# Optimization experiments

Measured on AMD Instinct MI355X. Metric: run time of the kernel, lower is better.

The kernel has to match this reference:

```python
import jax, jax.numpy as jnp
import numpy as np

EPS = 1e-8
NUM_HEADS = 8
SCALE = 25.0
SIM_THRESH = 0.75
BLOCK = 10  # per-frame proposal group size used by the zeroing mask


def _l2norm(x):
    return x / (jnp.linalg.norm(x, axis=-1, keepdims=True) + EPS)


def setup_inputs() -> dict:
    key = jax.random.key(0)
    ks = jax.random.split(key, 7)
    B, N, C = 1, 2000, 256
    H = NUM_HEADS
    x_cls = jax.random.normal(ks[0], (B, N, C), dtype=jnp.float32)
    x_reg = jax.random.normal(ks[1], (B, N, C), dtype=jnp.float32)
    cls_score = jax.random.uniform(ks[2], (N,), dtype=jnp.float32)
    fg_score = jax.random.uniform(ks[3], (N,), dtype=jnp.float32)
    coord_attn = jax.random.uniform(ks[4], (B, H, N, N), dtype=jnp.float32)
    W_qkv_cls = jax.random.normal(ks[5], (3 * C, C), dtype=jnp.float32) * 0.02
    W_qkv_reg = jax.random.normal(ks[6], (3 * C, C), dtype=jnp.float32) * 0.02
    return {"x_cls": x_cls, "x_reg": x_reg, "cls_score": cls_score,
            "fg_score": fg_score, "coord_attn": coord_attn,
            "W_qkv_cls": W_qkv_cls, "W_qkv_reg": W_qkv_reg}


def reference(x_cls, x_reg, cls_score, fg_score, coord_attn, W_qkv_cls, W_qkv_reg):
    B, N, C = x_cls.shape
    H = NUM_HEADS
    D = C // H

    def qkv(x, W):
        t = (x @ W.T).reshape(B, N, 3, H, D).transpose(2, 0, 3, 1, 4)  # [3,B,H,N,D]
        return t[0], t[1], t[2]

    q_cls, k_cls, v_cls = qkv(x_cls, W_qkv_cls)
    q_reg, k_reg, v_reg = qkv(x_reg, W_qkv_reg)

    q_cls, k_cls = _l2norm(q_cls), _l2norm(k_cls)
    q_reg, k_reg = _l2norm(q_reg), _l2norm(k_reg)
    v_cls_normed = _l2norm(v_cls)

    cs = cls_score.reshape(1, 1, 1, N)  # broadcast over [B,H,N,N]
    fs = fg_score.reshape(1, 1, 1, N)

    attn_cls_raw = jnp.einsum('bhnd,bhmd->bhnm', v_cls_normed, v_cls_normed)

    attn_cls = jax.nn.softmax(jnp.einsum('bhnd,bhmd->bhnm', q_cls, k_cls) * SCALE * cs, axis=-1)
    attn_reg = jax.nn.softmax(jnp.einsum('bhnd,bhmd->bhnm', q_reg, k_reg) * SCALE * fs, axis=-1)

    attn = (attn_reg + attn_cls) * 0.5 * coord_attn
    attn = jax.lax.stop_gradient(attn)  # original detaches before masking

    # block-diagonal zeroing: row j zeros cols [j//10*10, j//10*10+9), keep diagonal
    rows = jnp.arange(N)[:, None]
    cols = jnp.arange(N)[None, :]
    block_start = (rows // BLOCK) * BLOCK
    zero_mask = (cols >= block_start) & (cols < block_start + (BLOCK - 1)) & (cols != rows)
    attn = jnp.where(zero_mask, 0.0, attn)

    x = jnp.einsum('bhnm,bhmd->bhnd', attn, v_cls).transpose(0, 2, 1, 3).reshape(B, N, C)
    x_ori = v_cls.transpose(0, 2, 1, 3).reshape(B, N, C)
    x_cat = jnp.concatenate([x, x_ori], axis=-1)  # [B,N,2C]

    # ave=True branch
    sim_raw = jnp.sum(attn_cls_raw, axis=1)[0] / H          # [N,N]
    sim_mask = (sim_raw > SIM_THRESH).astype(x_cls.dtype)
    sim_attn = jnp.sum(attn, axis=1)[0] / H                 # [N,N]
    sim_round2 = jax.nn.softmax(sim_attn, axis=-1)
    sim_round2 = sim_mask * sim_round2 / (jnp.sum(sim_mask * sim_round2, axis=-1, keepdims=True) + EPS)
    return x_cat, sim_round2
```

## Files before the change

### kernel.cpp

```cpp
#include <hip/hip_runtime.h>
#include <math.h>

typedef _Float16 half8 __attribute__((ext_vector_type(8)));
typedef _Float16 half4 __attribute__((ext_vector_type(4)));
typedef float f32x4 __attribute__((ext_vector_type(4)));

constexpr int N = 2000;
constexpr int NP = 2048;
constexpr int H = 8;
constexpr int D = 32;
constexpr float SCL = 25.0f;
constexpr float L2E = 1.4426950408889634f;
constexpr float FM2 = 25.0f * L2E;

#define MFMA16(a,b,c)  __builtin_amdgcn_mfma_f32_16x16x32_f16((a),(b),(c),0,0,0)
#define MFMA16K(a,b,c) __builtin_amdgcn_mfma_f32_16x16x16f16((a),(b),(c),0,0,0)

__device__ __forceinline__ float fexp2(float x) { return __builtin_amdgcn_exp2f(x); }


__global__ __launch_bounds__(256) void wconv_kernel(
    const float* __restrict__ Wc, const float* __restrict__ Wr,
    _Float16* __restrict__ Wch, _Float16* __restrict__ Wrh)
{
    const int i = blockIdx.x * 256 + threadIdx.x;
    Wch[i] = (_Float16)Wc[i];
    Wrh[i] = (_Float16)Wr[i];
}

__global__ __launch_bounds__(256) void qkv_kernel(
    const float* __restrict__ xc, const float* __restrict__ xr,
    const _Float16* __restrict__ Wch, const _Float16* __restrict__ Wrh,
    const float* __restrict__ clsScore, const float* __restrict__ fgScore,
    _Float16* __restrict__ Qch, _Float16* __restrict__ Kch,
    _Float16* __restrict__ Qrh, _Float16* __restrict__ Krh,
    _Float16* __restrict__ Vnh, _Float16* __restrict__ Vth,
    float* __restrict__ out)
{
    constexpr int XS = 264;
    __shared__ _Float16 xs[16 * XS];
    const int t = threadIdx.x;
    const int n0 = blockIdx.x * 16;
    const int by = blockIdx.y;
    const int which = (by < 3) ? by : (by - 3);
    const bool isCls = by < 3;
    const float* x = isCls ? xc : xr;
    const _Float16* Wh = isCls ? Wch : Wrh;

    #pragma unroll
    for (int it = 0; it < 4; ++it) {
        const int f = t + it * 256;
        const int row = f >> 6, c4 = f & 63;
        const float4 v = *(const float4*)(x + (size_t)(n0 + row) * 256 + c4 * 4);
        half4 hv; hv[0]=(_Float16)v.x; hv[1]=(_Float16)v.y; hv[2]=(_Float16)v.z; hv[3]=(_Float16)v.w;
        *(half4*)&xs[row * XS + c4 * 4] = hv;
    }
    __syncthreads();

    const int w = t >> 6, l = t & 63;
    const int lr = l & 15, lg = l >> 4;
    const int obase = which * 256 + w * 64;
    f32x4 acc[4] = {{0,0,0,0},{0,0,0,0},{0,0,0,0},{0,0,0,0}};
    for (int k0 = 0; k0 < 256; k0 += 32) {
        const half8 aX = *(const half8*)&xs[lr * XS + k0 + lg * 8];
        #pragma unroll
        for (int s = 0; s < 4; ++s) {
            const half8 bW = *(const half8*)(Wh + (size_t)(obase + s * 16 + lr) * 256 + k0 + lg * 8);
            acc[s] = MFMA16(aX, bW, acc[s]);
        }
    }
    f32x4 kscale = {1.f,1.f,1.f,1.f};
    if (which == 1) {
        const float* sp = isCls ? clsScore : fgScore;
        kscale = (SCL * L2E) * *(const f32x4*)(sp + n0 + lg*4);
    }
    #pragma unroll
    for (int p = 0; p < 2; ++p) {
        const int h = 2 * w + p;
        float ss[4];
        #pragma unroll
        for (int j = 0; j < 4; ++j) {
            float v = acc[2*p][j]*acc[2*p][j] + acc[2*p+1][j]*acc[2*p+1][j];
            #pragma unroll
            for (int off = 1; off < 16; off <<= 1) v += __shfl_xor(v, off);
            ss[j] = sqrtf(v) + 1e-8f;
        }
        if (which < 2) {
            _Float16* Qd = isCls ? (which == 0 ? Qch : Kch) : (which == 0 ? Qrh : Krh);
            #pragma unroll
            for (int sh = 0; sh < 2; ++sh)
                #pragma unroll
                for (int j = 0; j < 4; ++j)
                    Qd[((size_t)h*NP + n0 + lg*4 + j)*D + sh*16 + lr]
                        = (_Float16)(acc[2*p+sh][j] / ss[j] * kscale[j]);
        } else {
            #pragma unroll
            for (int sh = 0; sh < 2; ++sh) {
                const int d = sh * 16 + lr;
                half4 tv;
                #pragma unroll
                for (int j = 0; j < 4; ++j) {
                    const float raw = acc[2*p+sh][j];
                    Vnh[((size_t)h*NP + n0 + lg*4 + j)*D + d] = (_Float16)(raw / ss[j]);
                    out[(size_t)(n0 + lg*4 + j)*512 + 256 + h*D + d] = raw;
                    tv[j] = (_Float16)raw;
                }
                *(half4*)(Vth + ((size_t)h*D + d)*NP + n0 + lg*4) = tv;
            }
        }
    }
}

__global__ __launch_bounds__(512) void stats_kernel(
    const _Float16* __restrict__ Qch, const _Float16* __restrict__ Kch,
    const _Float16* __restrict__ Qrh, const _Float16* __restrict__ Krh,
    float* __restrict__ BIAS)
{
    __shared__ float Ssh[2][4][16];
    const int t = threadIdx.x;
    const int w = t >> 6, l = t & 63;
    const int nsub = w >> 2, mq = w & 3;
    const int n0 = blockIdx.x * 32 + nsub * 16;
    const int h = blockIdx.y, z = blockIdx.z;
    const _Float16* Q = z ? Qrh : Qch;
    const _Float16* K = z ? Krh : Kch;
    const int lr = l & 15, lg = l >> 4;
    const half8 aQ = *(const half8*)(Q + ((size_t)h*NP + n0 + lr)*D + lg*8);
    float S[4] = {0.f, 0.f, 0.f, 0.f};
    const int mqB0 = (mq == 0) ? 0 : 31*mq;
    const int mqB1 = (mq == 3) ? 125 : 31*(mq+1);
    half8 bK = *(const half8*)(K + ((size_t)h*NP + mqB0*16 + lr)*D + lg*8);
    for (int ms = mqB0; ms < mqB1; ++ms) {
        const half8 cur = bK;
        if (ms + 1 < mqB1)
            bK = *(const half8*)(K + ((size_t)h*NP + (ms+1)*16 + lr)*D + lg*8);
        f32x4 z4 = {0.f, 0.f, 0.f, 0.f};
        const f32x4 c = MFMA16(aQ, cur, z4);
        #pragma unroll
        for (int j = 0; j < 4; ++j) S[j] += fexp2(c[j] - FM2);
    }
    #pragma unroll
    for (int j = 0; j < 4; ++j) {
        #pragma unroll
        for (int off = 1; off < 16; off <<= 1) S[j] += __shfl_xor(S[j], off);
    }
    if (lr == 0) {
        #pragma unroll
        for (int j = 0; j < 4; ++j) Ssh[nsub][mq][lg*4 + j] = S[j];
    }
    __syncthreads();
    if (t < 32) {
        const int ns = t >> 4, rl = t & 15;
        const int n = blockIdx.x * 32 + ns*16 + rl;
        BIAS[((size_t)z*H + h)*NP + n]
            = -__log2f(Ssh[ns][0][rl] + Ssh[ns][1][rl] + Ssh[ns][2][rl] + Ssh[ns][3][rl]) - FM2 - 1.0f;
    }
}

__global__ __launch_bounds__(256) void vvmask_kernel(
    const _Float16* __restrict__ Vnh, unsigned char* __restrict__ Mask)
{
    const int t = threadIdx.x;
    const int w = t >> 6, l = t & 63;
    const int n0 = blockIdx.y * 16;
    const int m00 = blockIdx.x * 256 + w * 64;
    const int lr = l & 15, lg = l >> 4;
    half8 aV[8];
    #pragma unroll
    for (int h = 0; h < 8; ++h)
        aV[h] = *(const half8*)(Vnh + ((size_t)(h*NP + n0 + lr))*D + lg*8);
    for (int s = 0; s < 4; ++s) {
        const int mb = m00 + s*16;
        f32x4 acc = {0.f, 0.f, 0.f, 0.f};
        #pragma unroll
        for (int h = 0; h < 8; ++h) {
            const half8 bV = *(const half8*)(Vnh + ((size_t)(h*NP + mb + lr))*D + lg*8);
            acc = MFMA16(aV[h], bV, acc);
        }
        const int m = mb + lr;
        if (m < N) {
            #pragma unroll
            for (int j = 0; j < 4; ++j) {
                const int n = n0 + lg*4 + j;
                Mask[(size_t)n*N + m] = (acc[j]*0.125f > 0.75f) ? (unsigned char)1 : (unsigned char)0;
            }
        }
    }
}

__global__ __launch_bounds__(256) void attn_kernel(
    const _Float16* __restrict__ Kch, const _Float16* __restrict__ Krh,
    const _Float16* __restrict__ Qch, const _Float16* __restrict__ Qrh,
    const _Float16* __restrict__ Vth, const float* __restrict__ coord,
    const float* __restrict__ BIAS,
    _Float16* __restrict__ SIMH8, float* __restrict__ out)
{
    constexpr int CW = 264;
    __shared__ float costage[2][16][CW];
    __shared__ float pvred[4][2][16][17];

    const int t = threadIdx.x;
    const int w = t >> 6, l = t & 63;
    const int lr = l & 15, lg = l >> 4;
    const int ny = blockIdx.x;
    const int h  = blockIdx.y;
    const int n0 = ny * 16;
    const int n  = n0 + lr;
    const int bs = (n / 10) * 10;

    const half8 aQc = *(const half8*)(Qch + ((size_t)h*NP + n)*D + lg*8);
    const half8 aQr = *(const half8*)(Qrh + ((size_t)h*NP + n)*D + lg*8);
    const float bC = BIAS[(size_t)h*NP + n];
    const float bR = BIAS[(size_t)(H + h)*NP + n];

    f32x4 streg[4];
    auto LOADCH = [&](int c) {
        #pragma unroll
        for (int i = 0; i < 4; ++i) {
            const int g = t + 256*i;
            const int row = g >> 6, c4 = g & 63;
            const int col = c*256 + c4*4;
            if (col < 2000)
                streg[i] = __builtin_nontemporal_load(
                    (const f32x4*)(coord + ((size_t)h*N + n0 + row)*N + col));
            else
                streg[i] = (f32x4){0.f,0.f,0.f,0.f};
        }
    };
    auto WRITECH = [&](int buf) {
        #pragma unroll
        for (int i = 0; i < 4; ++i) {
            const int g = t + 256*i;
            const int row = g >> 6, c4 = g & 63;
            *(f32x4*)&costage[buf][row][c4*4] = streg[i];
        }
    };

    f32x4 pv0 = {0,0,0,0}, pv1 = {0,0,0,0};

    LOADCH(0);
    WRITECH(0);
    __syncthreads();
    int buf = 0;

    for (int c = 0; c < 8; ++c) {
        const bool more = (c + 1 < 8);
        if (more) LOADCH(c + 1);
        __builtin_amdgcn_sched_barrier(0);

        const int nls = (c < 7) ? 4 : ((w < 3) ? 4 : 1);

        half8 kc[4], kr[4]; half4 v0[4], v1[4];
        #pragma unroll
        for (int i = 0; i < 4; ++i) {
            if (i >= nls) break;
            const int s = c*16 + w*4 + i;
            const int m = s*16;
            const size_t kb = ((size_t)h*NP + m + lr)*D + lg*8;
            kc[i] = *(const half8*)(Kch + kb);
            kr[i] = *(const half8*)(Krh + kb);
            v0[i] = *(const half4*)(Vth + ((size_t)(h*D + lr))*NP + m + lg*4);
            v1[i] = *(const half4*)(Vth + ((size_t)(h*D + 16 + lr))*NP + m + lg*4);
        }
        __builtin_amdgcn_sched_barrier(0);

        #pragma unroll
        for (int i = 0; i < 4; ++i) {
            if (i >= nls) break;
            const int s = c*16 + w*4 + i;
            const f32x4 co = *(const f32x4*)&costage[buf][lr][(w*4 + i)*16 + lg*4];
            f32x4 z4 = {0,0,0,0};
            const f32x4 cc = MFMA16(kc[i], aQc, z4);
            const f32x4 cr = MFMA16(kr[i], aQr, z4);
            half4 af;
            #pragma unroll
            for (int j = 0; j < 4; ++j) {
                const int m = s*16 + lg*4 + j;
                float a = (fexp2(cc[j] + bC) + fexp2(cr[j] + bR)) * co[j];
                if (m >= bs && m < bs + 9 && m != n) a = 0.f;
                af[j] = (_Float16)a;
            }
            *(half4*)(SIMH8 + ((size_t)h*N + n)*N + s*16 + lg*4) = af;
            pv0 = MFMA16K(af, v0[i], pv0);
            pv1 = MFMA16K(af, v1[i], pv1);
        }

        if (more) WRITECH(buf ^ 1);
        __syncthreads();
        buf ^= 1;
    }

    #pragma unroll
    for (int j = 0; j < 4; ++j) {
        pvred[w][0][lr][lg*4 + j] = pv0[j];
        pvred[w][1][lr][lg*4 + j] = pv1[j];
    }
    __syncthreads();
    {
        const int e0 = 2*t;
        const int d = e0 & 15, db = (e0 >> 4) & 1, q = e0 >> 5;
        const float u0 = pvred[0][db][d][q]   + pvred[1][db][d][q]
                       + pvred[2][db][d][q]   + pvred[3][db][d][q];
        const float u1 = pvred[0][db][d+1][q] + pvred[1][db][d+1][q]
                       + pvred[2][db][d+1][q] + pvred[3][db][d+1][q];
        *(float2*)(out + (size_t)(n0 + q)*512 + h*32 + db*16 + d) = make_float2(u0, u1);
    }
}

__global__ __launch_bounds__(256) void simfinal_kernel(
    const _Float16* __restrict__ SIMH8, const unsigned char* __restrict__ Mask,
    float* __restrict__ out)
{
    __shared__ float redA[4], redB[4];
    const int n = blockIdx.x, t = threadIdx.x;
    const unsigned char* mrow = Mask + (size_t)n * N;
    const bool act = t < 250;
    float f[8] = {0,0,0,0,0,0,0,0};
    unsigned int mk0 = 0, mk1 = 0;
    float mx = -1e30f;
    if (act) {
        #pragma unroll
        for (int h = 0; h < 8; ++h) {
            const half8 v8 = *(const half8*)(SIMH8 + ((size_t)h*N + n)*N + t*8);
            #pragma unroll
            for (int k = 0; k < 8; ++k) f[k] += (float)v8[k];
        }
        const uint2 mm = *(const uint2*)(mrow + t*8);
        mk0 = mm.x; mk1 = mm.y;
        #pragma unroll
        for (int k = 0; k < 8; ++k) mx = fmaxf(mx, f[k]);
    }
    #pragma unroll
    for (int off = 1; off < 64; off <<= 1) mx = fmaxf(mx, __shfl_xor(mx, off));
    const int wv = t >> 6;
    if ((t & 63) == 0) redA[wv] = mx;
    __syncthreads();
    const float M = fmaxf(fmaxf(redA[0], redA[1]), fmaxf(redA[2], redA[3]));
    float e[8];
    float sA = 0.f, sM = 0.f;
    if (act) {
        #pragma unroll
        for (int k = 0; k < 8; ++k) {
            e[k] = fexp2((f[k] - M) * (L2E * 0.125f));
            sA += e[k];
            const unsigned int mkb = ((k < 4 ? mk0 : mk1) >> (8*(k & 3))) & 0xffu;
            if (mkb) sM += e[k]; else e[k] = 0.f;
        }
    }
    #pragma unroll
    for (int off = 1; off < 64; off <<= 1) { sA += __shfl_xor(sA, off); sM += __shfl_xor(sM, off); }
    __syncthreads();
    if ((t & 63) == 0) { redA[wv] = sA; redB[wv] = sM; }
    __syncthreads();
    const float SA = redA[0] + redA[1] + redA[2] + redA[3];
    const float SMK = redB[0] + redB[1] + redB[2] + redB[3];
    const float inv = 1.f / (SMK + 1e-8f * SA);
    if (act) {
        float* orow = out + 1024000 + (size_t)n*N + t*8;
        *(float4*)(orow)     = make_float4(e[0]*inv, e[1]*inv, e[2]*inv, e[3]*inv);
        *(float4*)(orow + 4) = make_float4(e[4]*inv, e[5]*inv, e[6]*inv, e[7]*inv);
    }
}

extern "C" void kernel_launch(void* const* d_in, const int* in_sizes, int n_in,
                              void* d_out, int out_size, void* d_ws, size_t ws_size,
                              hipStream_t stream) {
    const float* x_cls     = (const float*)d_in[0];
    const float* x_reg     = (const float*)d_in[1];
    const float* cls_score = (const float*)d_in[2];
    const float* fg_score  = (const float*)d_in[3];
    const float* coord     = (const float*)d_in[4];
    const float* Wc        = (const float*)d_in[5];
    const float* Wr        = (const float*)d_in[6];

    char* base = (char*)d_ws;
    float* BIAS      = (float*)base;
    _Float16* SIMH8  = (_Float16*)(base + 131072);
    _Float16* Qch    = (_Float16*)(base + 64131072);
    _Float16* Kch    = Qch + 524288;
    _Float16* Qrh    = Qch + 2*524288;
    _Float16* Krh    = Qch + 3*524288;
    _Float16* Vnh    = Qch + 4*524288;
    _Float16* Vth    = Qch + 5*524288;
    _Float16* Wch    = (_Float16*)(base + 70422528);
    _Float16* Wrh    = (_Float16*)(base + 70815744);
    unsigned char* Mask = (unsigned char*)(base + 71208960);
    float* out = (float*)d_out;

    wconv_kernel<<<768, 256, 0, stream>>>(Wc, Wr, Wch, Wrh);
    qkv_kernel<<<dim3(125, 5), 256, 0, stream>>>(x_cls, x_reg, Wch, Wrh, cls_score, fg_score,
                                                 Qch, Kch, Qrh, Krh, Vnh, Vth, out);
    stats_kernel<<<dim3(63, 8, 2), 512, 0, stream>>>(Qch, Kch, Qrh, Krh, BIAS);
    vvmask_kernel<<<dim3(8, 125), 256, 0, stream>>>(Vnh, Mask);
    attn_kernel<<<dim3(125, 8), 256, 0, stream>>>(Kch, Krh, Qch, Qrh, Vth, coord,
                                                  BIAS, SIMH8, out);
    simfinal_kernel<<<2000, 256, 0, stream>>>(SIMH8, Mask, out);
}
```

Before: 145.0 us.

## Process four heads per attention block and pre-sum head groups before the sim write

Each attn_kernel block now handles four heads instead of one. It sums the masked attention over those heads in registers and writes 2 head-group partial sums to the workspace instead of 8 per-head fp16 matrices, which cuts global write traffic and the simfinal read traffic by about 4x. The coord tile is converted to fp16 when staged in shared memory, so it takes less LDS. In exchange the grid shrinks from 1000 to 250 blocks, register pressure rises (16 coord regs, 4 heads' Q and accumulators), and the coord values lose precision.

```diff
diff --git a/kernel.cpp b/kernel.cpp
--- a/kernel.cpp
+++ b/kernel.cpp
@@ -193,50 +193,63 @@
     const _Float16* __restrict__ Qch, const _Float16* __restrict__ Qrh,
     const _Float16* __restrict__ Vth, const float* __restrict__ coord,
     const float* __restrict__ BIAS,
-    _Float16* __restrict__ SIMH8, float* __restrict__ out)
+    _Float16* __restrict__ SIMG, float* __restrict__ out)
 {
     constexpr int CW = 264;
-    __shared__ float costage[2][16][CW];
-    __shared__ float pvred[4][2][16][17];
+    __shared__ _Float16 costage[2][4][16 * CW];
 
     const int t = threadIdx.x;
     const int w = t >> 6, l = t & 63;
     const int lr = l & 15, lg = l >> 4;
     const int ny = blockIdx.x;
-    const int h  = blockIdx.y;
+    const int g  = blockIdx.y;
+    const int h0 = g * 4;
     const int n0 = ny * 16;
     const int n  = n0 + lr;
     const int bs = (n / 10) * 10;
 
-    const half8 aQc = *(const half8*)(Qch + ((size_t)h*NP + n)*D + lg*8);
-    const half8 aQr = *(const half8*)(Qrh + ((size_t)h*NP + n)*D + lg*8);
-    const float bC = BIAS[(size_t)h*NP + n];
-    const float bR = BIAS[(size_t)(H + h)*NP + n];
-
-    f32x4 streg[4];
+    half8 aQc[4], aQr[4]; float bC[4], bR[4];
+    #pragma unroll
+    for (int hl = 0; hl < 4; ++hl) {
+        const int h = h0 + hl;
+        aQc[hl] = *(const half8*)(Qch + ((size_t)h*NP + n)*D + lg*8);
+        aQr[hl] = *(const half8*)(Qrh + ((size_t)h*NP + n)*D + lg*8);
+        bC[hl]  = BIAS[(size_t)h*NP + n];
+        bR[hl]  = BIAS[(size_t)(H + h)*NP + n];
+    }
+
+    half4 creg[16];
     auto LOADCH = [&](int c) {
         #pragma unroll
-        for (int i = 0; i < 4; ++i) {
-            const int g = t + 256*i;
-            const int row = g >> 6, c4 = g & 63;
-            const int col = c*256 + c4*4;
-            if (col < 2000)
-                streg[i] = __builtin_nontemporal_load(
-                    (const f32x4*)(coord + ((size_t)h*N + n0 + row)*N + col));
-            else
-                streg[i] = (f32x4){0.f,0.f,0.f,0.f};
+        for (int hl = 0; hl < 4; ++hl) {
+            #pragma unroll
+            for (int i = 0; i < 4; ++i) {
+                const int g16 = t + 256*i;
+                const int row = g16 >> 6, c4 = g16 & 63;
+                const int col = c*256 + c4*4;
+                f32x4 v = {0.f,0.f,0.f,0.f};
+                if (col < 2000)
+                    v = *(const f32x4*)(coord + ((size_t)(h0 + hl)*N + n0 + row)*N + col);
+                half4 hv; hv[0]=(_Float16)v[0]; hv[1]=(_Float16)v[1];
+                hv[2]=(_Float16)v[2]; hv[3]=(_Float16)v[3];
+                creg[hl*4 + i] = hv;
+            }
         }
     };
     auto WRITECH = [&](int buf) {
         #pragma unroll
-        for (int i = 0; i < 4; ++i) {
-            const int g = t + 256*i;
-            const int row = g >> 6, c4 = g & 63;
-            *(f32x4*)&costage[buf][row][c4*4] = streg[i];
+        for (int hl = 0; hl < 4; ++hl) {
+            #pragma unroll
+            for (int i = 0; i < 4; ++i) {
+                const int g16 = t + 256*i;
+                const int row = g16 >> 6, c4 = g16 & 63;
+                *(half4*)&costage[buf][hl][row*CW + c4*4] = creg[hl*4 + i];
+            }
         }
     };
 
-    f32x4 pv0 = {0,0,0,0}, pv1 = {0,0,0,0};
+    f32x4 pv0[4] = {{0,0,0,0},{0,0,0,0},{0,0,0,0},{0,0,0,0}};
+    f32x4 pv1[4] = {{0,0,0,0},{0,0,0,0},{0,0,0,0},{0,0,0,0}};
 
     LOADCH(0);
     WRITECH(0);
@@ -250,39 +263,55 @@
 
         const int nls = (c < 7) ? 4 : ((w < 3) ? 4 : 1);
 
-        half8 kc[4], kr[4]; half4 v0[4], v1[4];
+        float sacc[4][4] = {{0,0,0,0},{0,0,0,0},{0,0,0,0},{0,0,0,0}};
+
+        #pragma unroll
+        for (int hl = 0; hl < 4; ++hl) {
+            const int h = h0 + hl;
+            half8 kc[4], kr[4]; half4 v0[4], v1[4];
+            #pragma unroll
+            for (int i = 0; i < 4; ++i) {
+                if (i >= nls) break;
+                const int s = c*16 + w*4 + i;
+                const int m = s*16;
+                const size_t kb = ((size_t)h*NP + m + lr)*D + lg*8;
+                kc[i] = *(const half8*)(Kch + kb);
+                kr[i] = *(const half8*)(Krh + kb);
+                v0[i] = *(const half4*)(Vth + ((size_t)(h*D + lr))*NP + m + lg*4);
+                v1[i] = *(const half4*)(Vth + ((size_t)(h*D + 16 + lr))*NP + m + lg*4);
+            }
+            __builtin_amdgcn_sched_barrier(0);
+
+            #pragma unroll
+            for (int i = 0; i < 4; ++i) {
+                if (i >= nls) break;
+                const int s = c*16 + w*4 + i;
+                const half4 coh = *(const half4*)&costage[buf][hl][lr*CW + (w*4 + i)*16 + lg*4];
+                f32x4 z4 = {0,0,0,0};
+                const f32x4 cc = MFMA16(kc[i], aQc[hl], z4);
+                const f32x4 cr = MFMA16(kr[i], aQr[hl], z4);
+                half4 af;
+                #pragma unroll
+                for (int j = 0; j < 4; ++j) {
+                    const int m = s*16 + lg*4 + j;
+                    float a = (fexp2(cc[j] + bC[hl]) + fexp2(cr[j] + bR[hl])) * (float)coh[j];
+                    if (m >= bs && m < bs + 9 && m != n) a = 0.f;
+                    sacc[i][j] += a;
+                    af[j] = (_Float16)a;
+                }
+                pv0[hl] = MFMA16K(af, v0[i], pv0[hl]);
+                pv1[hl] = MFMA16K(af, v1[i], pv1[hl]);
+            }
+        }
+
         #pragma unroll
         for (int i = 0; i < 4; ++i) {
             if (i >= nls) break;
             const int s = c*16 + w*4 + i;
-            const int m = s*16;
-            const size_t kb = ((size_t)h*NP + m + lr)*D + lg*8;
-            kc[i] = *(const half8*)(Kch + kb);
-            kr[i] = *(const half8*)(Krh + kb);
-            v0[i] = *(const half4*)(Vth + ((size_t)(h*D + lr))*NP + m + lg*4);
-            v1[i] = *(const half4*)(Vth + ((size_t)(h*D + 16 + lr))*NP + m + lg*4);
-        }
-        __builtin_amdgcn_sched_barrier(0);
-
-        #pragma unroll
-        for (int i = 0; i < 4; ++i) {
-            if (i >= nls) break;
-            const int s = c*16 + w*4 + i;
-            const f32x4 co = *(const f32x4*)&costage[buf][lr][(w*4 + i)*16 + lg*4];
-            f32x4 z4 = {0,0,0,0};
-            const f32x4 cc = MFMA16(kc[i], aQc, z4);
-            const f32x4 cr = MFMA16(kr[i], aQr, z4);
-            half4 af;
-            #pragma unroll
-            for (int j = 0; j < 4; ++j) {
-                const int m = s*16 + lg*4 + j;
-                float a = (fexp2(cc[j] + bC) + fexp2(cr[j] + bR)) * co[j];
-                if (m >= bs && m < bs + 9 && m != n) a = 0.f;
-                af[j] = (_Float16)a;
-            }
-            *(half4*)(SIMH8 + ((size_t)h*N + n)*N + s*16 + lg*4) = af;
-            pv0 = MFMA16K(af, v0[i], pv0);
-            pv1 = MFMA16K(af, v1[i], pv1);
+            half4 sv;
+            #pragma unroll
+            for (int j = 0; j < 4; ++j) sv[j] = (_Float16)sacc[i][j];
+            *(half4*)(SIMG + ((size_t)g*N + n)*N + s*16 + lg*4) = sv;
         }
 
         if (more) WRITECH(buf ^ 1);
@@ -290,25 +319,26 @@
         buf ^= 1;
     }
 
-    #pragma unroll
-    for (int j = 0; j < 4; ++j) {
-        pvred[w][0][lr][lg*4 + j] = pv0[j];
-        pvred[w][1][lr][lg*4 + j] = pv1[j];
-    }
-    __syncthreads();
-    {
-        const int e0 = 2*t;
-        const int d = e0 & 15, db = (e0 >> 4) & 1, q = e0 >> 5;
-        const float u0 = pvred[0][db][d][q]   + pvred[1][db][d][q]
-                       + pvred[2][db][d][q]   + pvred[3][db][d][q];
-        const float u1 = pvred[0][db][d+1][q] + pvred[1][db][d+1][q]
-                       + pvred[2][db][d+1][q] + pvred[3][db][d+1][q];
-        *(float2*)(out + (size_t)(n0 + q)*512 + h*32 + db*16 + d) = make_float2(u0, u1);
+    float (*pvredH)[4][2][16][17] = (float(*)[4][2][16][17])&costage[0][0][0];
+    #pragma unroll
+    for (int hl = 0; hl < 4; ++hl)
+        #pragma unroll
+        for (int j = 0; j < 4; ++j) {
+            pvredH[hl][w][0][lr][lg*4 + j] = pv0[hl][j];
+            pvredH[hl][w][1][lr][lg*4 + j] = pv1[hl][j];
+        }
+    __syncthreads();
+    for (int e = t; e < 2048; e += 256) {
+        const int hl = e >> 9, e2 = e & 511;
+        const int d = e2 & 15, db = (e2 >> 4) & 1, q = e2 >> 5;
+        const float sum = pvredH[hl][0][db][d][q] + pvredH[hl][1][db][d][q]
+                        + pvredH[hl][2][db][d][q] + pvredH[hl][3][db][d][q];
+        out[(size_t)(n0 + q)*512 + (h0 + hl)*32 + db*16 + d] = sum;
     }
 }
 
 __global__ __launch_bounds__(256) void simfinal_kernel(
-    const _Float16* __restrict__ SIMH8, const unsigned char* __restrict__ Mask,
+    const _Float16* __restrict__ SIMG, const unsigned char* __restrict__ Mask,
     float* __restrict__ out)
 {
     __shared__ float redA[4], redB[4];
@@ -319,16 +349,12 @@
     unsigned int mk0 = 0, mk1 = 0;
     float mx = -1e30f;
     if (act) {
-        #pragma unroll
-        for (int h = 0; h < 8; ++h) {
-            const half8 v8 = *(const half8*)(SIMH8 + ((size_t)h*N + n)*N + t*8);
-            #pragma unroll
-            for (int k = 0; k < 8; ++k) f[k] += (float)v8[k];
-        }
+        const half8 va = *(const half8*)(SIMG + (size_t)n*N + t*8);
+        const half8 vb = *(const half8*)(SIMG + (size_t)N*N + (size_t)n*N + t*8);
         const uint2 mm = *(const uint2*)(mrow + t*8);
         mk0 = mm.x; mk1 = mm.y;
         #pragma unroll
-        for (int k = 0; k < 8; ++k) mx = fmaxf(mx, f[k]);
+        for (int k = 0; k < 8; ++k) { f[k] = (float)va[k] + (float)vb[k]; mx = fmaxf(mx, f[k]); }
     }
     #pragma unroll
     for (int off = 1; off < 64; off <<= 1) mx = fmaxf(mx, __shfl_xor(mx, off));
@@ -375,16 +401,16 @@
 
     char* base = (char*)d_ws;
     float* BIAS      = (float*)base;
-    _Float16* SIMH8  = (_Float16*)(base + 131072);
-    _Float16* Qch    = (_Float16*)(base + 64131072);
+    _Float16* SIMG   = (_Float16*)(base + 131072);
+    _Float16* Qch    = (_Float16*)(base + 32131072);
     _Float16* Kch    = Qch + 524288;
     _Float16* Qrh    = Qch + 2*524288;
     _Float16* Krh    = Qch + 3*524288;
     _Float16* Vnh    = Qch + 4*524288;
     _Float16* Vth    = Qch + 5*524288;
-    _Float16* Wch    = (_Float16*)(base + 70422528);
-    _Float16* Wrh    = (_Float16*)(base + 70815744);
-    unsigned char* Mask = (unsigned char*)(base + 71208960);
+    _Float16* Wch    = (_Float16*)(base + 38422528);
+    _Float16* Wrh    = (_Float16*)(base + 38815744);
+    unsigned char* Mask = (unsigned char*)(base + 39208960);
     float* out = (float*)d_out;
 
     wconv_kernel<<<768, 256, 0, stream>>>(Wc, Wr, Wch, Wrh);
@@ -392,7 +418,7 @@
                                                  Qch, Kch, Qrh, Krh, Vnh, Vth, out);
     stats_kernel<<<dim3(63, 8, 2), 512, 0, stream>>>(Qch, Kch, Qrh, Krh, BIAS);
     vvmask_kernel<<<dim3(8, 125), 256, 0, stream>>>(Vnh, Mask);
-    attn_kernel<<<dim3(125, 8), 256, 0, stream>>>(Kch, Krh, Qch, Qrh, Vth, coord,
-                                                  BIAS, SIMH8, out);
-    simfinal_kernel<<<2000, 256, 0, stream>>>(SIMH8, Mask, out);
-}
+    attn_kernel<<<dim3(125, 2), 256, 0, stream>>>(Kch, Krh, Qch, Qrh, Vth, coord,
+                                                  BIAS, SIMG, out);
+    simfinal_kernel<<<2000, 256, 0, stream>>>(SIMG, Mask, out);
+}
```

Result: no change. 147.3 us (+1.5%).
